# Kernel tuning notes

Measured on AMD Instinct MI355X. Metric: run time of the kernel, lower is better.

The kernel has to match this reference:

```python
import jax, jax.numpy as jnp
import numpy as np

B, C, H, W, K = 16, 64, 256, 256, 3

def setup_inputs() -> dict:
    key = jax.random.key(0)
    ks = jax.random.split(key, 3)
    x = jax.random.normal(ks[0], (B, C, H, W), dtype=jnp.float32)
    # ReDistribution params
    rd_k = jnp.ones((1, C, 1, 1), jnp.float32)
    rd_b = jnp.zeros((1, C, 1, 1), jnp.float32)
    # Spectral binary activation beta
    beta = jnp.ones((1,), jnp.float32)
    # HardBinaryConv real-valued latent weights (Conv2d default init scale)
    fan_in = C * K * K
    bound = 1.0 / np.sqrt(fan_in)
    conv_w = jax.random.uniform(ks[1], (C, C, K, K), jnp.float32, -bound, bound)
    # RPReLU params
    pr_bias0 = jnp.zeros((1, C, 1, 1), jnp.float32)
    prelu_w = jnp.full((C,), 0.25, jnp.float32)
    pr_bias1 = jnp.zeros((1, C, 1, 1), jnp.float32)
    return {"x": x, "rd_k": rd_k, "rd_b": rd_b, "beta": beta,
            "conv_w": conv_w, "pr_bias0": pr_bias0, "prelu_w": prelu_w,
            "pr_bias1": pr_bias1}

def _ste(hard, soft):
    # straight-through estimator: forward=hard, backward grads flow via soft
    return jax.lax.stop_gradient(hard - soft) + soft

def reference(x, rd_k, rd_b, beta, conv_w, pr_bias0, prelu_w, pr_bias1):
    sg = jax.lax.stop_gradient
    # ReDistribution
    out = x * rd_k + rd_b
    # Spectral binary activation with tanh STE
    out = _ste(jnp.sign(out), jnp.tanh(out * beta))
    # HardBinaryConv: per-output-channel mean |w| scaling, sign binarize, clip STE
    scaling = sg(jnp.mean(jnp.abs(conv_w), axis=(1, 2, 3), keepdims=True))  # [C,1,1,1]
    bw = _ste(scaling * jnp.sign(conv_w), jnp.clip(conv_w, -1.0, 1.0))
    y = jax.lax.conv_general_dilated(
        out, bw, window_strides=(1, 1), padding=((1, 1), (1, 1)),
        dimension_numbers=("NCHW", "OIHW", "NCHW"))
    # RPReLU: bias0 -> per-channel PReLU -> bias1
    y = y + pr_bias0
    y = jnp.where(y >= 0, y, prelu_w[None, :, None, None] * y)
    y = y + pr_bias1
    return y + x
```

## Files before the change

kernel.cpp:

```cpp
#include <hip/hip_runtime.h>
#include <cstdint>
#include <cstddef>

#define Bn 16
#define Cn 64
#define Hn 256
#define Wn 256
#define HWn (Hn * Wn)
#define TH 8
#define TW 128
#define ROWS (TH + 2)
#define COLS (TW + 2)
#define NBLK (Bn * (Hn / TH) * (Wn / TW))

typedef unsigned long long u64;
typedef float f32x4 __attribute__((ext_vector_type(4)));

__global__ __launch_bounds__(64) void pack_weights(const float* __restrict__ w,
                                                   const float* __restrict__ b0g,
                                                   const float* __restrict__ pwg,
                                                   const float* __restrict__ b1g,
                                                   u64* __restrict__ wbits,
                                                   float4* __restrict__ par,
                                                   int* __restrict__ corrx) {
    const int co = blockIdx.x;
    const int ci = threadIdx.x;
    const float* wp = w + ((size_t)co * Cn + ci) * 9;
    float v[9];
    float asum = 0.f;
    #pragma unroll
    for (int t = 0; t < 9; ++t) { v[t] = wp[t]; asum += fabsf(v[t]); }
    u64 m[9];
    #pragma unroll
    for (int t = 0; t < 9; ++t) m[t] = __ballot(v[t] > 0.f);
    #pragma unroll
    for (int off = 32; off; off >>= 1) asum += __shfl_xor(asum, off);
    if (ci == 0) {
        int c[9];
        #pragma unroll
        for (int t = 0; t < 9; ++t) {
            wbits[co * 9 + t] = m[t];
            c[t] = 64 - 2 * (int)__popcll(m[t]);
        }
        int* cx = corrx + co * 8;
        cx[0] = c[0] + c[1] + c[2];
        cx[1] = c[6] + c[7] + c[8];
        cx[2] = c[0] + c[3] + c[6];
        cx[3] = c[2] + c[5] + c[8];
        cx[4] = c[0]; cx[5] = c[2];
        cx[6] = c[6]; cx[7] = c[8];
        par[co] = make_float4(asum * (1.f / (Cn * 9)), b0g[co], pwg[co], b1g[co]);
    }
}

__global__ __launch_bounds__(256, 4) void fused(const float* __restrict__ x,
                                                const float* __restrict__ rdk,
                                                const float* __restrict__ rdb,
                                                const u64* __restrict__ wbits,
                                                const float4* __restrict__ par,
                                                const int* __restrict__ corrx,
                                                float* __restrict__ out) {
    __shared__ __align__(16) u64 s_a[ROWS][COLS];
    __shared__ float2 s_rd[Cn];

    const int tid = threadIdx.x;
    const int bid     = blockIdx.x;
    const int logical = (bid & 7) * (NBLK / 8) + (bid >> 3);
    const int n   = logical >> 6;
    const int rem = logical & 63;
    const int h0  = (rem >> 1) * TH;
    const int w0  = (rem & 1) * TW;

    if (tid < Cn) s_rd[tid] = make_float2(rdk[tid], rdb[tid]);
    __syncthreads();

    const float* xn = x + (size_t)n * Cn * HWn;
    for (int task = tid; task < 340; task += 256) {
        if (task < 320) {
            const int r = task >> 5;
            const int q = task & 31;
            const int gh = h0 - 1 + r;
            const int gw = w0 + 4 * q;
            u64 b0 = 0, b1 = 0, b2 = 0, b3 = 0;
            if (gh >= 0 && gh < Hn) {
                const float* xp = xn + (size_t)gh * Wn + gw;
                #pragma unroll 8
                for (int ci = 0; ci < Cn; ++ci) {
                    const float2 kb = s_rd[ci];
                    const f32x4 v = *reinterpret_cast<const f32x4*>(xp + (size_t)ci * HWn);
                    const u64 bit = 1ull << ci;
                    if (fmaf(v.x, kb.x, kb.y) > 0.f) b0 |= bit;
                    if (fmaf(v.y, kb.x, kb.y) > 0.f) b1 |= bit;
                    if (fmaf(v.z, kb.x, kb.y) > 0.f) b2 |= bit;
                    if (fmaf(v.w, kb.x, kb.y) > 0.f) b3 |= bit;
                }
            }
            s_a[r][1 + 4 * q] = b0;
            s_a[r][2 + 4 * q] = b1;
            s_a[r][3 + 4 * q] = b2;
            s_a[r][4 + 4 * q] = b3;
        } else {
            const int t2 = task - 320;
            const int r = t2 >> 1;
            const int side = t2 & 1;
            const int gh = h0 - 1 + r;
            const int gw = side ? (w0 + TW) : (w0 - 1);
            u64 b = 0;
            if (gh >= 0 && gh < Hn && gw >= 0 && gw < Wn) {
                const float* xp = xn + (size_t)gh * Wn + gw;
                #pragma unroll 8
                for (int ci = 0; ci < Cn; ++ci) {
                    const float2 kb = s_rd[ci];
                    if (fmaf(xp[(size_t)ci * HWn], kb.x, kb.y) > 0.f) b |= 1ull << ci;
                }
            }
            s_a[r][side ? (COLS - 1) : 0] = b;
        }
    }
    __syncthreads();

    const int r  = tid >> 5;
    const int c0 = (tid & 31) * 4;

    u64 A[3][6];
    #pragma unroll
    for (int dh = 0; dh < 3; ++dh)
        #pragma unroll
        for (int j = 0; j < 6; ++j)
            A[dh][j] = s_a[r + dh][c0 + j];
    #pragma unroll
    for (int dh = 0; dh < 3; ++dh)
        #pragma unroll
        for (int j = 0; j < 6; ++j)
            asm volatile("" : "+v"(A[dh][j]));

    const int gw0  = w0 + c0;
    const int h    = h0 + r;
    const int htop = (h == 0), hbot = (h == Hn - 1);
    const int wl   = (gw0 == 0), wr = (gw0 + 3 == Wn - 1);
    const int need = htop | hbot | wl | wr;

    const float* xp = x   + (size_t)n * Cn * HWn + (size_t)h * Wn + gw0;
    float*       op = out + (size_t)n * Cn * HWn + (size_t)h * Wn + gw0;

    auto conv1 = [&](int co, const f32x4& xv) {
        const u64* wb = wbits + co * 9;
        int is[4];
        #pragma unroll
        for (int p = 0; p < 4; ++p) {
            int acc = 0;
            #pragma unroll
            for (int dh = 0; dh < 3; ++dh) {
                acc += (int)__popcll(A[dh][p]     ^ wb[dh * 3]);
                acc += (int)__popcll(A[dh][p + 1] ^ wb[dh * 3 + 1]);
                acc += (int)__popcll(A[dh][p + 2] ^ wb[dh * 3 + 2]);
            }
            is[p] = 576 - 2 * acc;
        }
        if (need) {
            const int* cx = corrx + co * 8;
            const int sb = (htop ? cx[0] : 0) + (hbot ? cx[1] : 0);
            #pragma unroll
            for (int p = 0; p < 4; ++p) is[p] -= sb;
            if (wl) is[0] -= cx[2] - (htop ? cx[4] : 0) - (hbot ? cx[6] : 0);
            if (wr) is[3] -= cx[3] - (htop ? cx[5] : 0) - (hbot ? cx[7] : 0);
        }
        const float4 p4 = par[co];
        f32x4 o;
        #pragma unroll
        for (int j = 0; j < 4; ++j) {
            float y = fmaf(p4.x, (float)is[j], p4.y);
            y = (y >= 0.f) ? y : y * p4.z;
            o[j] = y + p4.w + xv[j];
        }
        __builtin_nontemporal_store(o, reinterpret_cast<f32x4*>(op + (size_t)co * HWn));
    };

    f32x4 xva = *reinterpret_cast<const f32x4*>(xp);
    f32x4 xvb = *reinterpret_cast<const f32x4*>(xp + HWn);
    for (int co = 0; co < Cn; co += 2) {
        const int pfa = (co + 2 < Cn) ? co + 2 : co;
        const f32x4 na = *reinterpret_cast<const f32x4*>(xp + (size_t)pfa * HWn);
        conv1(co, xva);
        xva = na;
        const int pfb = (co + 3 < Cn) ? co + 3 : co + 1;
        const f32x4 nb = *reinterpret_cast<const f32x4*>(xp + (size_t)pfb * HWn);
        conv1(co + 1, xvb);
        xvb = nb;
    }
}

extern "C" void kernel_launch(void* const* d_in, const int* in_sizes, int n_in,
                              void* d_out, int out_size, void* d_ws, size_t ws_size,
                              hipStream_t stream) {
    const float* x      = (const float*)d_in[0];
    const float* rd_k   = (const float*)d_in[1];
    const float* rd_b   = (const float*)d_in[2];
    const float* conv_w = (const float*)d_in[4];
    const float* pb0    = (const float*)d_in[5];
    const float* pw     = (const float*)d_in[6];
    const float* pb1    = (const float*)d_in[7];
    float* out = (float*)d_out;

    uint8_t* ws = (uint8_t*)d_ws;
    u64*    wbits = (u64*)ws;
    float4* par   = (float4*)(ws + 4608);
    int*    corrx = (int*)(ws + 4608 + 1024);

    pack_weights<<<Cn, 64, 0, stream>>>(conv_w, pb0, pw, pb1, wbits, par, corrx);
    fused<<<NBLK, 256, 0, stream>>>(x, rd_k, rd_b, wbits, par, corrx, out);
}
```

Baseline: 164.4 us.

## Halve tile width, two pixels per thread, reload activations from LDS per channel group

Tile width drops from 128 to 64, doubling the block count. Each thread now computes 2 output pixels instead of 4, and the launch bound moves to 8 blocks per SM. Activation bit-vectors are no longer held in registers for the whole channel loop; they are reloaded from shared memory as 128-bit vector loads for every group of 4 output channels, and the x loads for the residual are batched per group. The aim is lower register pressure and higher occupancy to hide memory latency. The costs are more halo overhead in the binarization stage, repeated LDS traffic, and narrower 8-byte stores.

```diff
diff --git a/kernel.cpp b/kernel.cpp
--- a/kernel.cpp
+++ b/kernel.cpp
@@ -8,12 +8,14 @@
 #define Wn 256
 #define HWn (Hn * Wn)
 #define TH 8
-#define TW 128
+#define TW 64
 #define ROWS (TH + 2)
 #define COLS (TW + 2)
 #define NBLK (Bn * (Hn / TH) * (Wn / TW))
 
 typedef unsigned long long u64;
+typedef u64   u64x2 __attribute__((ext_vector_type(2)));
+typedef float f32x2 __attribute__((ext_vector_type(2)));
 typedef float f32x4 __attribute__((ext_vector_type(4)));
 
 __global__ __launch_bounds__(64) void pack_weights(const float* __restrict__ w,
@@ -53,7 +55,7 @@
     }
 }
 
-__global__ __launch_bounds__(256, 4) void fused(const float* __restrict__ x,
+__global__ __launch_bounds__(256, 8) void fused(const float* __restrict__ x,
                                                 const float* __restrict__ rdk,
                                                 const float* __restrict__ rdb,
                                                 const u64* __restrict__ wbits,
@@ -66,19 +68,19 @@
     const int tid = threadIdx.x;
     const int bid     = blockIdx.x;
     const int logical = (bid & 7) * (NBLK / 8) + (bid >> 3);
-    const int n   = logical >> 6;
-    const int rem = logical & 63;
-    const int h0  = (rem >> 1) * TH;
-    const int w0  = (rem & 1) * TW;
+    const int n   = logical >> 7;
+    const int rem = logical & 127;
+    const int h0  = (rem >> 2) * TH;
+    const int w0  = (rem & 3) * TW;
 
     if (tid < Cn) s_rd[tid] = make_float2(rdk[tid], rdb[tid]);
     __syncthreads();
 
     const float* xn = x + (size_t)n * Cn * HWn;
-    for (int task = tid; task < 340; task += 256) {
-        if (task < 320) {
-            const int r = task >> 5;
-            const int q = task & 31;
+    if (tid < 180) {
+        if (tid < 160) {
+            const int r = tid >> 4;
+            const int q = tid & 15;
             const int gh = h0 - 1 + r;
             const int gw = w0 + 4 * q;
             u64 b0 = 0, b1 = 0, b2 = 0, b3 = 0;
@@ -100,7 +102,7 @@
             s_a[r][3 + 4 * q] = b2;
             s_a[r][4 + 4 * q] = b3;
         } else {
-            const int t2 = task - 320;
+            const int t2 = tid - 160;
             const int r = t2 >> 1;
             const int side = t2 & 1;
             const int gh = h0 - 1 + r;
@@ -119,74 +121,63 @@
     }
     __syncthreads();
 
-    const int r  = tid >> 5;
-    const int c0 = (tid & 31) * 4;
-
-    u64 A[3][6];
-    #pragma unroll
-    for (int dh = 0; dh < 3; ++dh)
-        #pragma unroll
-        for (int j = 0; j < 6; ++j)
-            A[dh][j] = s_a[r + dh][c0 + j];
-    #pragma unroll
-    for (int dh = 0; dh < 3; ++dh)
-        #pragma unroll
-        for (int j = 0; j < 6; ++j)
-            asm volatile("" : "+v"(A[dh][j]));
-
-    const int gw0  = w0 + c0;
-    const int h    = h0 + r;
+    const int r   = tid >> 5;
+    const int c0  = (tid & 31) * 2;
+    const int gw0 = w0 + c0;
+    const int h   = h0 + r;
     const int htop = (h == 0), hbot = (h == Hn - 1);
-    const int wl   = (gw0 == 0), wr = (gw0 + 3 == Wn - 1);
+    const int wl = (gw0 == 0), wr = (gw0 + 1 == Wn - 1);
     const int need = htop | hbot | wl | wr;
 
     const float* xp = x   + (size_t)n * Cn * HWn + (size_t)h * Wn + gw0;
     float*       op = out + (size_t)n * Cn * HWn + (size_t)h * Wn + gw0;
 
-    auto conv1 = [&](int co, const f32x4& xv) {
-        const u64* wb = wbits + co * 9;
-        int is[4];
-        #pragma unroll
-        for (int p = 0; p < 4; ++p) {
-            int acc = 0;
+    const u64* ap = &s_a[r][c0];
+    for (int co0 = 0; co0 < Cn; co0 += 4) {
+        asm volatile("" : "+v"(ap));
+        u64 A[3][4];
+        #pragma unroll
+        for (int dh = 0; dh < 3; ++dh) {
+            const u64x2 t0 = *reinterpret_cast<const u64x2*>(ap + dh * COLS);
+            const u64x2 t1 = *reinterpret_cast<const u64x2*>(ap + dh * COLS + 2);
+            A[dh][0] = t0.x; A[dh][1] = t0.y; A[dh][2] = t1.x; A[dh][3] = t1.y;
+        }
+        f32x2 xq[4];
+        #pragma unroll
+        for (int j = 0; j < 4; ++j)
+            xq[j] = *reinterpret_cast<const f32x2*>(xp + (size_t)(co0 + j) * HWn);
+
+        #pragma unroll
+        for (int j = 0; j < 4; ++j) {
+            const int co = co0 + j;
+            const u64* wb = wbits + co * 9;
+            int a0 = 0, a1 = 0;
             #pragma unroll
             for (int dh = 0; dh < 3; ++dh) {
-                acc += (int)__popcll(A[dh][p]     ^ wb[dh * 3]);
-                acc += (int)__popcll(A[dh][p + 1] ^ wb[dh * 3 + 1]);
-                acc += (int)__popcll(A[dh][p + 2] ^ wb[dh * 3 + 2]);
-            }
-            is[p] = 576 - 2 * acc;
-        }
-        if (need) {
-            const int* cx = corrx + co * 8;
-            const int sb = (htop ? cx[0] : 0) + (hbot ? cx[1] : 0);
-            #pragma unroll
-            for (int p = 0; p < 4; ++p) is[p] -= sb;
-            if (wl) is[0] -= cx[2] - (htop ? cx[4] : 0) - (hbot ? cx[6] : 0);
-            if (wr) is[3] -= cx[3] - (htop ? cx[5] : 0) - (hbot ? cx[7] : 0);
-        }
-        const float4 p4 = par[co];
-        f32x4 o;
-        #pragma unroll
-        for (int j = 0; j < 4; ++j) {
-            float y = fmaf(p4.x, (float)is[j], p4.y);
-            y = (y >= 0.f) ? y : y * p4.z;
-            o[j] = y + p4.w + xv[j];
-        }
-        __builtin_nontemporal_store(o, reinterpret_cast<f32x4*>(op + (size_t)co * HWn));
-    };
-
-    f32x4 xva = *reinterpret_cast<const f32x4*>(xp);
-    f32x4 xvb = *reinterpret_cast<const f32x4*>(xp + HWn);
-    for (int co = 0; co < Cn; co += 2) {
-        const int pfa = (co + 2 < Cn) ? co + 2 : co;
-        const f32x4 na = *reinterpret_cast<const f32x4*>(xp + (size_t)pfa * HWn);
-        conv1(co, xva);
-        xva = na;
-        const int pfb = (co + 3 < Cn) ? co + 3 : co + 1;
-        const f32x4 nb = *reinterpret_cast<const f32x4*>(xp + (size_t)pfb * HWn);
-        conv1(co + 1, xvb);
-        xvb = nb;
+                const u64 q0 = wb[dh * 3], q1 = wb[dh * 3 + 1], q2 = wb[dh * 3 + 2];
+                a0 += (int)__popcll(A[dh][0] ^ q0) + (int)__popcll(A[dh][1] ^ q1)
+                    + (int)__popcll(A[dh][2] ^ q2);
+                a1 += (int)__popcll(A[dh][1] ^ q0) + (int)__popcll(A[dh][2] ^ q1)
+                    + (int)__popcll(A[dh][3] ^ q2);
+            }
+            int is0 = 576 - 2 * a0, is1 = 576 - 2 * a1;
+
+            if (need) {
+                const int* cx = corrx + co * 8;
+                const int sb = (htop ? cx[0] : 0) + (hbot ? cx[1] : 0);
+                is0 -= sb; is1 -= sb;
+                if (wl) is0 -= cx[2] - (htop ? cx[4] : 0) - (hbot ? cx[6] : 0);
+                if (wr) is1 -= cx[3] - (htop ? cx[5] : 0) - (hbot ? cx[7] : 0);
+            }
+
+            const float4 p4 = par[co];
+            float y0 = fmaf(p4.x, (float)is0, p4.y);
+            y0 = (y0 >= 0.f) ? y0 : y0 * p4.z;
+            float y1 = fmaf(p4.x, (float)is1, p4.y);
+            y1 = (y1 >= 0.f) ? y1 : y1 * p4.z;
+            f32x2 o = { y0 + p4.w + xq[j].x, y1 + p4.w + xq[j].y };
+            __builtin_nontemporal_store(o, reinterpret_cast<f32x2*>(op + (size_t)co * HWn));
+        }
     }
 }
 
```

After: 204.7 us. 24.6% more time.

## Tile full image rows per block and reload packed activations from LDS per channel group

Applied to the files above, without the earlier changes.

Blocks now cover the full 256-pixel width of 8 rows with 512 threads, which removes the per-tile left/right halo columns. Those columns are replaced by zeroed padding entries, so the serial single-pixel halo packing tasks go away. The conv loop now re-reads the 3x6 packed activation window from LDS with 16-byte vector loads for every group of 4 output channels, instead of keeping it in registers across all channels. It also loads the 4 residual x vectors per group up front rather than prefetching one channel ahead. The aim is less register pressure and less redundant halo work, at the cost of more LDS traffic, a larger shared-memory footprint and fewer, bigger blocks.

```diff
diff --git a/kernel.cpp b/kernel.cpp
--- a/kernel.cpp
+++ b/kernel.cpp
@@ -8,12 +8,13 @@
 #define Wn 256
 #define HWn (Hn * Wn)
 #define TH 8
-#define TW 128
 #define ROWS (TH + 2)
-#define COLS (TW + 2)
-#define NBLK (Bn * (Hn / TH) * (Wn / TW))
+#define COLS (Wn + 2)
+#define NBLK (Bn * (Hn / TH))
+#define THREADS 512
 
 typedef unsigned long long u64;
+typedef u64   u64x2 __attribute__((ext_vector_type(2)));
 typedef float f32x4 __attribute__((ext_vector_type(4)));
 
 __global__ __launch_bounds__(64) void pack_weights(const float* __restrict__ w,
@@ -53,140 +54,122 @@
     }
 }
 
-__global__ __launch_bounds__(256, 4) void fused(const float* __restrict__ x,
-                                                const float* __restrict__ rdk,
-                                                const float* __restrict__ rdb,
-                                                const u64* __restrict__ wbits,
-                                                const float4* __restrict__ par,
-                                                const int* __restrict__ corrx,
-                                                float* __restrict__ out) {
+__global__ __launch_bounds__(THREADS, 4) void fused(const float* __restrict__ x,
+                                                    const float* __restrict__ rdk,
+                                                    const float* __restrict__ rdb,
+                                                    const u64* __restrict__ wbits,
+                                                    const float4* __restrict__ par,
+                                                    const int* __restrict__ corrx,
+                                                    float* __restrict__ out) {
     __shared__ __align__(16) u64 s_a[ROWS][COLS];
     __shared__ float2 s_rd[Cn];
 
     const int tid = threadIdx.x;
     const int bid     = blockIdx.x;
     const int logical = (bid & 7) * (NBLK / 8) + (bid >> 3);
-    const int n   = logical >> 6;
-    const int rem = logical & 63;
-    const int h0  = (rem >> 1) * TH;
-    const int w0  = (rem & 1) * TW;
+    const int n  = logical >> 5;
+    const int h0 = (logical & 31) * TH;
 
     if (tid < Cn) s_rd[tid] = make_float2(rdk[tid], rdb[tid]);
+    if (tid < 2 * ROWS) s_a[tid >> 1][(tid & 1) ? (COLS - 1) : 0] = 0;
     __syncthreads();
 
     const float* xn = x + (size_t)n * Cn * HWn;
-    for (int task = tid; task < 340; task += 256) {
-        if (task < 320) {
-            const int r = task >> 5;
-            const int q = task & 31;
-            const int gh = h0 - 1 + r;
-            const int gw = w0 + 4 * q;
-            u64 b0 = 0, b1 = 0, b2 = 0, b3 = 0;
-            if (gh >= 0 && gh < Hn) {
-                const float* xp = xn + (size_t)gh * Wn + gw;
-                #pragma unroll 8
-                for (int ci = 0; ci < Cn; ++ci) {
-                    const float2 kb = s_rd[ci];
-                    const f32x4 v = *reinterpret_cast<const f32x4*>(xp + (size_t)ci * HWn);
-                    const u64 bit = 1ull << ci;
-                    if (fmaf(v.x, kb.x, kb.y) > 0.f) b0 |= bit;
-                    if (fmaf(v.y, kb.x, kb.y) > 0.f) b1 |= bit;
-                    if (fmaf(v.z, kb.x, kb.y) > 0.f) b2 |= bit;
-                    if (fmaf(v.w, kb.x, kb.y) > 0.f) b3 |= bit;
-                }
+    for (int task = tid; task < 640; task += THREADS) {
+        const int r  = task >> 6;
+        const int q  = task & 63;
+        const int gh = h0 - 1 + r;
+        const int gw = 4 * q;
+        u64 b0 = 0, b1 = 0, b2 = 0, b3 = 0;
+        if (gh >= 0 && gh < Hn) {
+            const float* xp = xn + (size_t)gh * Wn + gw;
+            #pragma unroll 8
+            for (int ci = 0; ci < Cn; ++ci) {
+                const float2 kb = s_rd[ci];
+                const f32x4 v = *reinterpret_cast<const f32x4*>(xp + (size_t)ci * HWn);
+                const u64 bit = 1ull << ci;
+                if (fmaf(v.x, kb.x, kb.y) > 0.f) b0 |= bit;
+                if (fmaf(v.y, kb.x, kb.y) > 0.f) b1 |= bit;
+                if (fmaf(v.z, kb.x, kb.y) > 0.f) b2 |= bit;
+                if (fmaf(v.w, kb.x, kb.y) > 0.f) b3 |= bit;
             }
-            s_a[r][1 + 4 * q] = b0;
-            s_a[r][2 + 4 * q] = b1;
-            s_a[r][3 + 4 * q] = b2;
-            s_a[r][4 + 4 * q] = b3;
-        } else {
-            const int t2 = task - 320;
-            const int r = t2 >> 1;
-            const int side = t2 & 1;
-            const int gh = h0 - 1 + r;
-            const int gw = side ? (w0 + TW) : (w0 - 1);
-            u64 b = 0;
-            if (gh >= 0 && gh < Hn && gw >= 0 && gw < Wn) {
-                const float* xp = xn + (size_t)gh * Wn + gw;
-                #pragma unroll 8
-                for (int ci = 0; ci < Cn; ++ci) {
-                    const float2 kb = s_rd[ci];
-                    if (fmaf(xp[(size_t)ci * HWn], kb.x, kb.y) > 0.f) b |= 1ull << ci;
-                }
-            }
-            s_a[r][side ? (COLS - 1) : 0] = b;
         }
+        s_a[r][1 + gw] = b0;
+        s_a[r][2 + gw] = b1;
+        s_a[r][3 + gw] = b2;
+        s_a[r][4 + gw] = b3;
     }
     __syncthreads();
 
-    const int r  = tid >> 5;
-    const int c0 = (tid & 31) * 4;
-
-    u64 A[3][6];
-    #pragma unroll
-    for (int dh = 0; dh < 3; ++dh)
-        #pragma unroll
-        for (int j = 0; j < 6; ++j)
-            A[dh][j] = s_a[r + dh][c0 + j];
-    #pragma unroll
-    for (int dh = 0; dh < 3; ++dh)
-        #pragma unroll
-        for (int j = 0; j < 6; ++j)
-            asm volatile("" : "+v"(A[dh][j]));
-
-    const int gw0  = w0 + c0;
-    const int h    = h0 + r;
+    const int r  = tid >> 6;
+    const int c0 = (tid & 63) * 4;
+    const int h  = h0 + r;
     const int htop = (h == 0), hbot = (h == Hn - 1);
-    const int wl   = (gw0 == 0), wr = (gw0 + 3 == Wn - 1);
+    const int wl = (c0 == 0), wr = (c0 + 3 == Wn - 1);
     const int need = htop | hbot | wl | wr;
 
-    const float* xp = x   + (size_t)n * Cn * HWn + (size_t)h * Wn + gw0;
-    float*       op = out + (size_t)n * Cn * HWn + (size_t)h * Wn + gw0;
+    const float* xp = x   + (size_t)n * Cn * HWn + (size_t)h * Wn + c0;
+    float*       op = out + (size_t)n * Cn * HWn + (size_t)h * Wn + c0;
 
-    auto conv1 = [&](int co, const f32x4& xv) {
-        const u64* wb = wbits + co * 9;
-        int is[4];
+    const u64* ap = &s_a[r][c0];
+    for (int co0 = 0; co0 < Cn; co0 += 4) {
+        asm volatile("" : "+v"(ap));
+        u64 A[3][6];
         #pragma unroll
-        for (int p = 0; p < 4; ++p) {
-            int acc = 0;
+        for (int dh = 0; dh < 3; ++dh) {
+            const u64x2 t0 = *reinterpret_cast<const u64x2*>(ap + dh * COLS);
+            const u64x2 t1 = *reinterpret_cast<const u64x2*>(ap + dh * COLS + 2);
+            const u64x2 t2 = *reinterpret_cast<const u64x2*>(ap + dh * COLS + 4);
+            A[dh][0] = t0.x; A[dh][1] = t0.y; A[dh][2] = t1.x;
+            A[dh][3] = t1.y; A[dh][4] = t2.x; A[dh][5] = t2.y;
+        }
+        #pragma unroll
+        for (int dh = 0; dh < 3; ++dh)
             #pragma unroll
-            for (int dh = 0; dh < 3; ++dh) {
-                acc += (int)__popcll(A[dh][p]     ^ wb[dh * 3]);
-                acc += (int)__popcll(A[dh][p + 1] ^ wb[dh * 3 + 1]);
-                acc += (int)__popcll(A[dh][p + 2] ^ wb[dh * 3 + 2]);
-            }
-            is[p] = 576 - 2 * acc;
-        }
-        if (need) {
-            const int* cx = corrx + co * 8;
-            const int sb = (htop ? cx[0] : 0) + (hbot ? cx[1] : 0);
-            #pragma unroll
-            for (int p = 0; p < 4; ++p) is[p] -= sb;
-            if (wl) is[0] -= cx[2] - (htop ? cx[4] : 0) - (hbot ? cx[6] : 0);
-            if (wr) is[3] -= cx[3] - (htop ? cx[5] : 0) - (hbot ? cx[7] : 0);
-        }
-        const float4 p4 = par[co];
-        f32x4 o;
+            for (int j = 0; j < 6; ++j)
+                asm volatile("" : "+v"(A[dh][j]));
+
+        f32x4 xq[4];
+        #pragma unroll
+        for (int j = 0; j < 4; ++j)
+            xq[j] = *reinterpret_cast<const f32x4*>(xp + (size_t)(co0 + j) * HWn);
+
         #pragma unroll
         for (int j = 0; j < 4; ++j) {
-            float y = fmaf(p4.x, (float)is[j], p4.y);
-            y = (y >= 0.f) ? y : y * p4.z;
-            o[j] = y + p4.w + xv[j];
+            const int co = co0 + j;
+            const u64* wb = wbits + co * 9;
+            int is[4];
+            #pragma unroll
+            for (int p = 0; p < 4; ++p) {
+                int acc = 0;
+                #pragma unroll
+                for (int dh = 0; dh < 3; ++dh) {
+                    acc += (int)__popcll(A[dh][p]     ^ wb[dh * 3]);
+                    acc += (int)__popcll(A[dh][p + 1] ^ wb[dh * 3 + 1]);
+                    acc += (int)__popcll(A[dh][p + 2] ^ wb[dh * 3 + 2]);
+                }
+                is[p] = 576 - 2 * acc;
+            }
+
+            if (need) {
+                const int* cx = corrx + co * 8;
+                const int sb = (htop ? cx[0] : 0) + (hbot ? cx[1] : 0);
+                #pragma unroll
+                for (int p = 0; p < 4; ++p) is[p] -= sb;
+                if (wl) is[0] -= cx[2] - (htop ? cx[4] : 0) - (hbot ? cx[6] : 0);
+                if (wr) is[3] -= cx[3] - (htop ? cx[5] : 0) - (hbot ? cx[7] : 0);
+            }
+
+            const float4 p4 = par[co];
+            f32x4 o;
+            #pragma unroll
+            for (int p = 0; p < 4; ++p) {
+                float y = fmaf(p4.x, (float)is[p], p4.y);
+                y = (y >= 0.f) ? y : y * p4.z;
+                o[p] = y + p4.w + xq[j][p];
+            }
+            __builtin_nontemporal_store(o, reinterpret_cast<f32x4*>(op + (size_t)co * HWn));
         }
-        __builtin_nontemporal_store(o, reinterpret_cast<f32x4*>(op + (size_t)co * HWn));
-    };
-
-    f32x4 xva = *reinterpret_cast<const f32x4*>(xp);
-    f32x4 xvb = *reinterpret_cast<const f32x4*>(xp + HWn);
-    for (int co = 0; co < Cn; co += 2) {
-        const int pfa = (co + 2 < Cn) ? co + 2 : co;
-        const f32x4 na = *reinterpret_cast<const f32x4*>(xp + (size_t)pfa * HWn);
-        conv1(co, xva);
-        xva = na;
-        const int pfb = (co + 3 < Cn) ? co + 3 : co + 1;
-        const f32x4 nb = *reinterpret_cast<const f32x4*>(xp + (size_t)pfb * HWn);
-        conv1(co + 1, xvb);
-        xvb = nb;
     }
 }
 
@@ -208,5 +191,5 @@
     int*    corrx = (int*)(ws + 4608 + 1024);
 
     pack_weights<<<Cn, 64, 0, stream>>>(conv_w, pb0, pw, pb1, wbits, par, corrx);
-    fused<<<NBLK, 256, 0, stream>>>(x, rd_k, rd_b, wbits, par, corrx, out);
+    fused<<<NBLK, THREADS, 0, stream>>>(x, rd_k, rd_b, wbits, par, corrx, out);
 }
```

After: 160.2 us. 1.03x faster.
